# Kernel optimization log

Measured on AMD Instinct MI355X. Metric: run time of the kernel, lower is better.

The kernel has to match this reference:

```python
import jax, jax.numpy as jnp
import numpy as np

LN_EPS = 1e-5

def _layernorm(x, g, b):
    mu = jnp.mean(x, axis=-1, keepdims=True)
    var = jnp.mean(jnp.square(x - mu), axis=-1, keepdims=True)
    return (x - mu) * jax.lax.rsqrt(var + LN_EPS) * g + b

def setup_inputs() -> dict:
    key = jax.random.key(0)
    B, T, C = 8, 2048, 1024
    ks = jax.random.split(key, 16)
    s = 1.0 / np.sqrt(C)
    inp = {
        'x':   jax.random.normal(ks[0], (B, T, C), dtype=jnp.float32),
        'Wq':  jax.random.uniform(ks[1], (C, C), jnp.float32, -s, s),
        'bq':  jax.random.uniform(ks[2], (C,), jnp.float32, -s, s),
        'Wk':  jax.random.uniform(ks[3], (C, C), jnp.float32, -s, s),
        'bk':  jax.random.uniform(ks[4], (C,), jnp.float32, -s, s),
        'Wv':  jax.random.uniform(ks[5], (C, C), jnp.float32, -s, s),
        'bv':  jax.random.uniform(ks[6], (C,), jnp.float32, -s, s),
        'g1':  jnp.ones((C,), jnp.float32),
        'be1': jnp.zeros((C,), jnp.float32),
        'W1':  jax.random.uniform(ks[7], (C, C), jnp.float32, -s, s),
        'bf1': jax.random.uniform(ks[8], (C,), jnp.float32, -s, s),
        'W2':  jax.random.uniform(ks[9], (C, C), jnp.float32, -s, s),
        'bf2': jax.random.uniform(ks[10], (C,), jnp.float32, -s, s),
        'g2':  jnp.ones((C,), jnp.float32),
        'be2': jnp.zeros((C,), jnp.float32),
    }
    return inp

def reference(x, Wq, bq, Wk, bk, Wv, bv, g1, be1, W1, bf1, W2, bf2, g2, be2):
    B, T, C = x.shape
    q = x @ Wq + bq
    k = x @ Wk + bk
    v = x @ Wv + bv
    # FFT cross-correlation along time axis
    fq = jnp.fft.rfft(q, axis=1)
    fk = jnp.fft.rfft(k, axis=1)
    corr = jnp.fft.irfft(fq * jnp.conj(fk), n=T, axis=1)  # [B,T,C]
    weights = jax.nn.softmax(corr, axis=1)
    # einsum 'btd,btv->btd': weights * sum over v's channel dim
    attn = weights * jnp.sum(v, axis=-1, keepdims=True)
    x = _layernorm(x + attn, g1, be1)
    h = jax.nn.relu(x @ W1 + bf1) @ W2 + bf2
    x = _layernorm(x + h, g2, be2)
    return x
```

## Files before the change

kernel.cpp:

```cpp
#include <hip/hip_runtime.h>
#include <math.h>

#define B_DIM 8
#define T_DIM 2048
#define C_DIM 1024
#define BT_DIM (B_DIM * T_DIM)
#define FSZ ((size_t)BT_DIM * C_DIM)
#define LN_EPS 1e-5f

typedef __bf16 bf16x8 __attribute__((ext_vector_type(8)));
typedef _Float16 f16x8 __attribute__((ext_vector_type(8)));
typedef float f32x4 __attribute__((ext_vector_type(4)));

__device__ __forceinline__ unsigned short f2bf(float f) {
  __bf16 h = (__bf16)f;
  return __builtin_bit_cast(unsigned short, h);
}
__device__ __forceinline__ unsigned short f2h(float f) {
  _Float16 h = (_Float16)f;
  return __builtin_bit_cast(unsigned short, h);
}
__device__ __forceinline__ float bf2f(unsigned short u) {
  unsigned int v = ((unsigned int)u) << 16;
  return __builtin_bit_cast(float, v);
}

__device__ __forceinline__ void gld16(const void* g, void* l) {
  __builtin_amdgcn_global_load_lds(
      (const __attribute__((address_space(1))) unsigned int*)g,
      (__attribute__((address_space(3))) unsigned int*)l, 16, 0, 0);
}

__device__ __forceinline__ int swz(int a) {
  return a ^ (((a >> 4) ^ (a >> 8)) & 15);
}

__device__ __forceinline__ int enc11(int f) {
  return ((f & 3) << 9) | (((f >> 2) & 3) << 7) | (((f >> 4) & 3) << 5) |
         (((f >> 6) & 3) << 3) | (((f >> 8) & 3) << 1) | ((f >> 10) & 1);
}

__global__ __launch_bounds__(256)
void cvt_split_sv_kernel(const float* __restrict__ x, const float* __restrict__ wvsum,
                         const float* __restrict__ bvsum,
                         unsigned short* __restrict__ hi, unsigned short* __restrict__ lo,
                         float* __restrict__ sv) {
  const int r = blockIdx.x;
  const int tid = threadIdx.x;
  const size_t base = (size_t)r * C_DIM + (tid << 2);
  float4 v = *(const float4*)(x + base);
  float4 w = *(const float4*)(wvsum + (tid << 2));
  float f[4] = {v.x, v.y, v.z, v.w};
  unsigned short hv[4], lv[4];
#pragma unroll
  for (int i = 0; i < 4; i++) {
    _Float16 hb = (_Float16)f[i];
    hv[i] = __builtin_bit_cast(unsigned short, hb);
    lv[i] = f2h(f[i] - (float)hb);
  }
  *(ushort4*)(hi + base) = make_ushort4(hv[0], hv[1], hv[2], hv[3]);
  *(ushort4*)(lo + base) = make_ushort4(lv[0], lv[1], lv[2], lv[3]);
  float s = v.x * w.x + v.y * w.y + v.z * w.z + v.w * w.w;
#pragma unroll
  for (int off = 32; off > 0; off >>= 1) s += __shfl_down(s, off);
  __shared__ float ps[4];
  if ((tid & 63) == 0) ps[tid >> 6] = s;
  __syncthreads();
  if (tid == 0) sv[r] = ps[0] + ps[1] + ps[2] + ps[3] + bvsum[0];
}

__global__ __launch_bounds__(256)
void wtrans_f16_kernel(const float* __restrict__ W, unsigned short* __restrict__ Wt,
                       int K, int N) {
  __shared__ float tile[32][33];
  const int tid = threadIdx.x;
  const int tx = tid & 31, ty = tid >> 5;
  const int n0 = blockIdx.x * 32, k0 = blockIdx.y * 32;
#pragma unroll
  for (int i = 0; i < 4; i++) {
    int row = ty + i * 8;
    tile[row][tx] = W[(size_t)(k0 + row) * N + n0 + tx];
  }
  __syncthreads();
#pragma unroll
  for (int i = 0; i < 4; i++) {
    int row = ty + i * 8;
    Wt[(size_t)(n0 + row) * K + k0 + tx] = f2h(tile[tx][row]);
  }
}

__global__ __launch_bounds__(256)
void wtrans_kernel(const float* __restrict__ W, unsigned short* __restrict__ Wt,
                   int K, int N) {
  __shared__ float tile[32][33];
  const int tid = threadIdx.x;
  const int tx = tid & 31, ty = tid >> 5;
  const int n0 = blockIdx.x * 32, k0 = blockIdx.y * 32;
#pragma unroll
  for (int i = 0; i < 4; i++) {
    int row = ty + i * 8;
    tile[row][tx] = W[(size_t)(k0 + row) * N + n0 + tx];
  }
  __syncthreads();
#pragma unroll
  for (int i = 0; i < 4; i++) {
    int row = ty + i * 8;
    Wt[(size_t)(n0 + row) * K + k0 + tx] = f2bf(tile[tx][row]);
  }
}

__global__ __launch_bounds__(256)
void wv_rowsum_kernel(const float* __restrict__ Wv, const float* __restrict__ bv,
                      float* __restrict__ wvsum, float* __restrict__ bvsum) {
  const int r = blockIdx.x;
  const int tid = threadIdx.x;
  const float* src = (r < C_DIM) ? (Wv + (size_t)r * C_DIM) : bv;
  float4 t4 = *(const float4*)(src + (tid << 2));
  float s = t4.x + t4.y + t4.z + t4.w;
#pragma unroll
  for (int off = 32; off > 0; off >>= 1) s += __shfl_down(s, off);
  __shared__ float ps[4];
  if ((tid & 63) == 0) ps[tid >> 6] = s;
  __syncthreads();
  if (tid == 0) {
    float v = ps[0] + ps[1] + ps[2] + ps[3];
    if (r < C_DIM) wvsum[r] = v; else bvsum[0] = v;
  }
}

__global__ __launch_bounds__(256, 2)
void gemm_bf16_kernel(const __bf16* __restrict__ A, const __bf16* __restrict__ Bt,
                      const float* __restrict__ bias, float* Yf, unsigned short* Yb,
                      int K, int N, int do_relu) {
  __shared__ __align__(16) __bf16 As[128 * 32];
  __shared__ __align__(16) __bf16 Bs[128 * 32];
  const int tid = threadIdx.x;
  const int wave = tid >> 6, lane = tid & 63;
  const int wr = wave >> 1, wc = wave & 1;
  const int r15 = lane & 15, kq = lane >> 4;
  const int h = blockIdx.y * 8 + blockIdx.x;
  const int xcd = h & 7, s = h >> 3;
  const int mIdx = (xcd << 4) + (s & 7) + ((s >> 6) << 3);
  const int nIdx = (s >> 3) & 7;
  const int m0 = mIdx * 128, n0 = nIdx * 128;

  f32x4 acc[4][4] = {};

  for (int k0 = 0; k0 < K; k0 += 32) {
#pragma unroll
    for (int r = 0; r < 2; ++r) {
      int idx = r * 256 + tid;
      int row = idx >> 2;
      int ko = (idx & 3) ^ ((row >> 1) & 3);
      gld16(A + (size_t)(m0 + row) * K + k0 + ko * 8, &As[idx * 8]);
      gld16(Bt + (size_t)(n0 + row) * K + k0 + ko * 8, &Bs[idx * 8]);
    }
    __syncthreads();
    bf16x8 afr[4], bfr[4];
#pragma unroll
    for (int i = 0; i < 4; i++) {
      int ar = wr * 64 + i * 16 + r15;
      afr[i] = *(const bf16x8*)&As[(ar * 4 + (kq ^ ((ar >> 1) & 3))) * 8];
      int br = wc * 64 + i * 16 + r15;
      bfr[i] = *(const bf16x8*)&Bs[(br * 4 + (kq ^ ((br >> 1) & 3))) * 8];
    }
#pragma unroll
    for (int mi = 0; mi < 4; mi++)
#pragma unroll
      for (int ni = 0; ni < 4; ni++)
        acc[mi][ni] = __builtin_amdgcn_mfma_f32_16x16x32_bf16(afr[mi], bfr[ni], acc[mi][ni], 0, 0, 0);
    __syncthreads();
  }

  float bv[4];
#pragma unroll
  for (int ni = 0; ni < 4; ni++) bv[ni] = bias[n0 + wc * 64 + ni * 16 + r15];

#pragma unroll
  for (int mi = 0; mi < 4; mi++)
#pragma unroll
    for (int ni = 0; ni < 4; ni++) {
      const int n = n0 + wc * 64 + ni * 16 + r15;
#pragma unroll
      for (int r = 0; r < 4; r++) {
        const int m = m0 + wr * 64 + mi * 16 + kq * 4 + r;
        float v = acc[mi][ni][r] + bv[ni];
        if (do_relu) v = fmaxf(v, 0.f);
        if (Yf) Yf[(size_t)m * N + n] = v;
        if (Yb) Yb[(size_t)m * N + n] = f2bf(v);
      }
    }
}

__global__ __launch_bounds__(512, 2)
void gemm_qkT_f16_8ph_kernel(const _Float16* __restrict__ Ahi, const _Float16* __restrict__ Alo,
                             const _Float16* __restrict__ Bq, const _Float16* __restrict__ Bk,
                             const float* __restrict__ biasq, const float* __restrict__ biask,
                             float* __restrict__ Yq, float* __restrict__ Yk, int K, int N) {
  __shared__ __align__(16) _Float16 AhL[3][256 * 32];
  __shared__ __align__(16) _Float16 AlL[3][256 * 32];
  __shared__ __align__(16) _Float16 BqL[3][128 * 32];
  __shared__ __align__(16) _Float16 BkL[3][128 * 32];

  const int tid = threadIdx.x;
  const int wave = tid >> 6, lane = tid & 63;
  const int wr = wave >> 2, wc = wave & 3;
  const int r15 = lane & 15, kq = lane >> 4;
  const int h = blockIdx.y * 8 + blockIdx.x;
  const int xcd = h & 7, s = h >> 3;
  const int mIdx = (xcd << 3) + (s & 3) + ((s >> 5) << 2);
  const int nIdx = (s >> 2) & 7;
  const int m0 = mIdx * 256, n0 = nIdx * 128;
  const int NT = K >> 5;

  const int row_a0 = tid >> 2;
  const int row_a1 = row_a0 + 128;
  const int ch = tid & 3;
  const int ko0 = ch ^ ((row_a0 >> 1) & 3);
  const int ko1 = ch ^ ((row_a1 >> 1) & 3);
  const _Float16* agh0 = Ahi + (size_t)(m0 + row_a0) * K + ko0 * 8;
  const _Float16* agl0 = Alo + (size_t)(m0 + row_a0) * K + ko0 * 8;
  const _Float16* agh1 = Ahi + (size_t)(m0 + row_a1) * K + ko1 * 8;
  const _Float16* agl1 = Alo + (size_t)(m0 + row_a1) * K + ko1 * 8;
  const _Float16* bgq  = Bq  + (size_t)(n0 + row_a0) * K + ko0 * 8;
  const _Float16* bgk  = Bk  + (size_t)(n0 + row_a0) * K + ko0 * 8;

  const int ksel = kq ^ ((r15 >> 1) & 3);
  const int aoff = (wr * 128 + r15) * 32 + ksel * 8;
  const int boff = (wc * 32 + r15) * 32 + ksel * 8;

  f32x4 accq[8][2] = {};
  f32x4 acck[8][2] = {};

  gld16(agh0 + 0, &AhL[0][(size_t)tid * 8]);
  gld16(agl0 + 0, &AlL[0][(size_t)tid * 8]);
  gld16(agh1 + 0, &AhL[0][(size_t)(tid + 512) * 8]);
  gld16(agl1 + 0, &AlL[0][(size_t)(tid + 512) * 8]);
  gld16(bgq + 0, &BqL[0][(size_t)tid * 8]);
  gld16(bgk + 0, &BkL[0][(size_t)tid * 8]);
  gld16(agh0 + 32, &AhL[1][(size_t)tid * 8]);
  gld16(agl0 + 32, &AlL[1][(size_t)tid * 8]);
  gld16(agh1 + 32, &AhL[1][(size_t)(tid + 512) * 8]);
  gld16(agl1 + 32, &AlL[1][(size_t)(tid + 512) * 8]);
  gld16(bgq + 32, &BqL[1][(size_t)tid * 8]);
  gld16(bgk + 32, &BkL[1][(size_t)tid * 8]);

  int bR = 0;
  int bS = 2;

  for (int j = 0; j < NT; ++j) {
    if (j < NT - 1) {
      asm volatile("s_waitcnt vmcnt(6)" ::: "memory");
    } else {
      asm volatile("s_waitcnt vmcnt(0)" ::: "memory");
    }
    __builtin_amdgcn_s_barrier();
    __builtin_amdgcn_sched_barrier(0);

    const int kk = (j + 2) * 32;
    const bool doStage = (j + 2 < NT);

    f16x8 bqf[2], bkf[2];
#pragma unroll
    for (int ni = 0; ni < 2; ++ni) {
      bqf[ni] = *(const f16x8*)&BqL[bR][boff + ni * 512];
      bkf[ni] = *(const f16x8*)&BkL[bR][boff + ni * 512];
    }

#pragma unroll
    for (int p = 0; p < 4; ++p) {
      f16x8 ah0 = *(const f16x8*)&AhL[bR][aoff + (2 * p + 0) * 512];
      f16x8 al0 = *(const f16x8*)&AlL[bR][aoff + (2 * p + 0) * 512];
      f16x8 ah1 = *(const f16x8*)&AhL[bR][aoff + (2 * p + 1) * 512];
      f16x8 al1 = *(const f16x8*)&AlL[bR][aoff + (2 * p + 1) * 512];
      if (doStage) {
        if (p == 0) {
          gld16(agh0 + kk, &AhL[bS][(size_t)tid * 8]);
          gld16(agl0 + kk, &AlL[bS][(size_t)tid * 8]);
        }
        if (p == 1) {
          gld16(agh1 + kk, &AhL[bS][(size_t)(tid + 512) * 8]);
          gld16(agl1 + kk, &AlL[bS][(size_t)(tid + 512) * 8]);
        }
        if (p == 2) gld16(bgq + kk, &BqL[bS][(size_t)tid * 8]);
        if (p == 3) gld16(bgk + kk, &BkL[bS][(size_t)tid * 8]);
      }
      __builtin_amdgcn_s_barrier();
      asm volatile("s_waitcnt lgkmcnt(0)" ::: "memory");
      __builtin_amdgcn_sched_barrier(0);
      __builtin_amdgcn_s_setprio(1);
#pragma unroll
      for (int m2 = 0; m2 < 2; ++m2) {
        const int mi = 2 * p + m2;
        const f16x8 ahv = m2 ? ah1 : ah0;
        const f16x8 alv = m2 ? al1 : al0;
#pragma unroll
        for (int ni = 0; ni < 2; ++ni) {
          accq[mi][ni] = __builtin_amdgcn_mfma_f32_16x16x32_f16(ahv, bqf[ni], accq[mi][ni], 0, 0, 0);
          accq[mi][ni] = __builtin_amdgcn_mfma_f32_16x16x32_f16(alv, bqf[ni], accq[mi][ni], 0, 0, 0);
          acck[mi][ni] = __builtin_amdgcn_mfma_f32_16x16x32_f16(ahv, bkf[ni], acck[mi][ni], 0, 0, 0);
          acck[mi][ni] = __builtin_amdgcn_mfma_f32_16x16x32_f16(alv, bkf[ni], acck[mi][ni], 0, 0, 0);
        }
      }
      __builtin_amdgcn_s_setprio(0);
      __builtin_amdgcn_sched_barrier(0);
    }

    bR = (bR + 1 == 3) ? 0 : bR + 1;
    bS = (bS + 1 == 3) ? 0 : bS + 1;
  }

  float bvq[2], bvk[2];
#pragma unroll
  for (int ni = 0; ni < 2; ++ni) {
    bvq[ni] = biasq[n0 + wc * 32 + ni * 16 + r15];
    bvk[ni] = biask[n0 + wc * 32 + ni * 16 + r15];
  }

#pragma unroll
  for (int mi = 0; mi < 8; ++mi) {
    const int mbase = m0 + wr * 128 + mi * 16 + kq * 4;
    const int bb = mbase >> 11;
    const int t = mbase & (T_DIM - 1);
#pragma unroll
    for (int ni = 0; ni < 2; ++ni) {
      const int n = n0 + wc * 32 + ni * 16 + r15;
      const size_t o = ((size_t)bb * C_DIM + n) * T_DIM + t;
      *(float4*)(Yq + o) = make_float4(accq[mi][ni][0] + bvq[ni], accq[mi][ni][1] + bvq[ni],
                                       accq[mi][ni][2] + bvq[ni], accq[mi][ni][3] + bvq[ni]);
      *(float4*)(Yk + o) = make_float4(acck[mi][ni][0] + bvk[ni], acck[mi][ni][1] + bvk[ni],
                                       acck[mi][ni][2] + bvk[ni], acck[mi][ni][3] + bvk[ni]);
    }
  }
}

__device__ void fft_dif(float2* X, const float2* tw, int tid, float sgn) {
#pragma unroll
  for (int s = 0; s < 5; s++) {
    const int m = 512 >> (2 * s);
    const int jstep = 512 / m;
#pragma unroll
    for (int ii = 0; ii < 2; ii++) {
      const int i = tid + ii * 256;
      const int q = i & (m - 1);
      const int a0 = ((i - q) << 2) + q;
      float2 x0 = X[swz(a0)];
      float2 x1 = X[swz(a0 + m)];
      float2 x2 = X[swz(a0 + 2 * m)];
      float2 x3 = X[swz(a0 + 3 * m)];
      float2 t0 = make_float2(x0.x + x2.x, x0.y + x2.y);
      float2 t2 = make_float2(x0.x - x2.x, x0.y - x2.y);
      float2 t1 = make_float2(x1.x + x3.x, x1.y + x3.y);
      float2 t3 = make_float2(x1.x - x3.x, x1.y - x3.y);
      const float jx = -sgn * t3.y, jy = sgn * t3.x;
      float2 y0 = make_float2(t0.x + t1.x, t0.y + t1.y);
      float2 y1 = make_float2(t2.x + jx, t2.y + jy);
      float2 y2 = make_float2(t0.x - t1.x, t0.y - t1.y);
      float2 y3 = make_float2(t2.x - jx, t2.y - jy);
      const int j1 = q * jstep;
      float2 tv = tw[swz(j1)];
      const float c1 = tv.x, s1 = tv.y * sgn;
      const float c2 = c1 * c1 - s1 * s1, s2 = 2.f * c1 * s1;
      const float c3 = c2 * c1 - s2 * s1, s3 = c2 * s1 + s2 * c1;
      X[swz(a0)] = y0;
      X[swz(a0 + m)] = make_float2(c1 * y1.x - s1 * y1.y, c1 * y1.y + s1 * y1.x);
      X[swz(a0 + 2 * m)] = make_float2(c2 * y2.x - s2 * y2.y, c2 * y2.y + s2 * y2.x);
      X[swz(a0 + 3 * m)] = make_float2(c3 * y3.x - s3 * y3.y, c3 * y3.y + s3 * y3.x);
    }
    __syncthreads();
  }
#pragma unroll
  for (int ii = 0; ii < 4; ii++) {
    const int a = (tid + ii * 256) << 1;
    float2 u = X[swz(a)], v = X[swz(a + 1)];
    X[swz(a)] = make_float2(u.x + v.x, u.y + v.y);
    X[swz(a + 1)] = make_float2(u.x - v.x, u.y - v.y);
  }
  __syncthreads();
}

__device__ void fft_dit_inv(float2* X, const float2* tw, int tid) {
#pragma unroll
  for (int ii = 0; ii < 4; ii++) {
    const int a = (tid + ii * 256) << 1;
    float2 u = X[swz(a)], v = X[swz(a + 1)];
    X[swz(a)] = make_float2(u.x + v.x, u.y + v.y);
    X[swz(a + 1)] = make_float2(u.x - v.x, u.y - v.y);
  }
  __syncthreads();
#pragma unroll
  for (int s = 4; s >= 0; s--) {
    const int m = 512 >> (2 * s);
    const int jstep = 512 / m;
#pragma unroll
    for (int ii = 0; ii < 2; ii++) {
      const int i = tid + ii * 256;
      const int q = i & (m - 1);
      const int a0 = ((i - q) << 2) + q;
      float2 v0 = X[swz(a0)];
      float2 v1 = X[swz(a0 + m)];
      float2 v2 = X[swz(a0 + 2 * m)];
      float2 v3 = X[swz(a0 + 3 * m)];
      const int j1 = q * jstep;
      float2 tv = tw[swz(j1)];
      const float c1 = tv.x, s1 = tv.y;
      const float c2 = c1 * c1 - s1 * s1, s2 = 2.f * c1 * s1;
      const float c3 = c2 * c1 - s2 * s1, s3 = c2 * s1 + s2 * c1;
      float2 w1 = make_float2(c1 * v1.x - s1 * v1.y, c1 * v1.y + s1 * v1.x);
      float2 w2 = make_float2(c2 * v2.x - s2 * v2.y, c2 * v2.y + s2 * v2.x);
      float2 w3 = make_float2(c3 * v3.x - s3 * v3.y, c3 * v3.y + s3 * v3.x);
      float2 t0 = make_float2(v0.x + w2.x, v0.y + w2.y);
      float2 t2 = make_float2(v0.x - w2.x, v0.y - w2.y);
      float2 t1 = make_float2(w1.x + w3.x, w1.y + w3.y);
      float2 t3 = make_float2(w1.x - w3.x, w1.y - w3.y);
      const float jx = -t3.y, jy = t3.x;
      X[swz(a0)] = make_float2(t0.x + t1.x, t0.y + t1.y);
      X[swz(a0 + m)] = make_float2(t2.x + jx, t2.y + jy);
      X[swz(a0 + 2 * m)] = make_float2(t0.x - t1.x, t0.y - t1.y);
      X[swz(a0 + 3 * m)] = make_float2(t2.x - jx, t2.y - jy);
    }
    __syncthreads();
  }
}

__global__ __launch_bounds__(256)
void corr_fft_kernel(const float* qT, const float* kT, unsigned short* __restrict__ wT,
                     float* __restrict__ Iv) {
  __shared__ float2 bA[2048];
  __shared__ float2 bB[2048];
  __shared__ float2 tw[512];
  __shared__ float2 red[4];
  const int tid = threadIdx.x;
  const int wave = tid >> 6, lane = tid & 63;
  const int b = blockIdx.y;
  const int c0 = blockIdx.x * 2;
  const float* q0 = qT + ((size_t)b * C_DIM + c0) * T_DIM;
  const float* k0p = kT + ((size_t)b * C_DIM + c0) * T_DIM;

#pragma unroll
  for (int jj = 0; jj < 2; jj++) {
    int j = tid + jj * 256;
    float sA, cA;
    __sincosf((float)j * (6.283185307179586f / 2048.0f), &sA, &cA);
    tw[swz(j)] = make_float2(cA, sA);
  }

#pragma unroll
  for (int jj = 0; jj < 8; jj++) {
    int t = tid + jj * 256;
    bA[swz(t)] = make_float2(q0[t], q0[t + T_DIM]);
    bB[swz(t)] = make_float2(k0p[t], k0p[t + T_DIM]);
  }
  __syncthreads();

  fft_dif(bA, tw, tid, -1.0f);
  fft_dif(bB, tw, tid, -1.0f);

#pragma unroll 1
  for (int f = tid; f <= 1024; f += 256) {
    const int g = (2048 - f) & 2047;
    const int p = swz(enc11(f));
    const int p2 = swz(enc11(g));
    float2 Zq = bA[p], Zq2 = bA[p2];
    float2 Zk = bB[p], Zk2 = bB[p2];
    float2 Aq = make_float2(0.5f * (Zq.x + Zq2.x), 0.5f * (Zq.y - Zq2.y));
    float2 Dq = make_float2(Zq.x - Zq2.x, Zq.y + Zq2.y);
    float2 Bq = make_float2(0.5f * Dq.y, -0.5f * Dq.x);
    float2 Ak = make_float2(0.5f * (Zk.x + Zk2.x), 0.5f * (Zk.y - Zk2.y));
    float2 Dk = make_float2(Zk.x - Zk2.x, Zk.y + Zk2.y);
    float2 Bk = make_float2(0.5f * Dk.y, -0.5f * Dk.x);
    float2 G = make_float2(Aq.x * Ak.x + Aq.y * Ak.y, Aq.y * Ak.x - Aq.x * Ak.y);
    float2 H = make_float2(Bq.x * Bk.x + Bq.y * Bk.y, Bq.y * Bk.x - Bq.x * Bk.y);
    bA[p] = make_float2(G.x - H.y, G.y + H.x);
    if (p2 != p) bA[p2] = make_float2(G.x + H.y, -G.y + H.x);
  }
  __syncthreads();

  fft_dit_inv(bA, tw, tid);

  unsigned short* o0 = wT + ((size_t)b * C_DIM + c0) * T_DIM;
  const float sc = 1.0f / 2048.0f;
  float mx0 = -INFINITY, mx1 = -INFINITY;
#pragma unroll
  for (int jj = 0; jj < 8; jj++) {
    int t = tid + jj * 256;
    float2 o = bA[swz(t)];
    mx0 = fmaxf(mx0, o.x);
    mx1 = fmaxf(mx1, o.y);
  }
#pragma unroll
  for (int off = 32; off > 0; off >>= 1) {
    mx0 = fmaxf(mx0, __shfl_down(mx0, off));
    mx1 = fmaxf(mx1, __shfl_down(mx1, off));
  }
  if (lane == 0) red[wave] = make_float2(mx0, mx1);
  __syncthreads();
  const float M0 = fmaxf(fmaxf(red[0].x, red[1].x), fmaxf(red[2].x, red[3].x));
  const float M1 = fmaxf(fmaxf(red[0].y, red[1].y), fmaxf(red[2].y, red[3].y));
  __syncthreads();
  float s0 = 0.f, s1 = 0.f;
#pragma unroll
  for (int jj = 0; jj < 8; jj++) {
    int t = tid + jj * 256;
    float2 o = bA[swz(t)];
    float e0 = __expf((o.x - M0) * sc);
    float e1 = __expf((o.y - M1) * sc);
    s0 += e0;
    s1 += e1;
    o0[t] = f2bf(e0);
    o0[t + T_DIM] = f2bf(e1);
  }
#pragma unroll
  for (int off = 32; off > 0; off >>= 1) {
    s0 += __shfl_down(s0, off);
    s1 += __shfl_down(s1, off);
  }
  if (lane == 0) red[wave] = make_float2(s0, s1);
  __syncthreads();
  if (tid == 0) {
    float S0 = red[0].x + red[1].x + red[2].x + red[3].x;
    float S1 = red[0].y + red[1].y + red[2].y + red[3].y;
    Iv[(size_t)b * C_DIM + c0] = 1.0f / S0;
    Iv[(size_t)b * C_DIM + c0 + 1] = 1.0f / S1;
  }
}

__global__ __launch_bounds__(512)
void attn_ln_kernel(const unsigned short* __restrict__ wT, const float* __restrict__ Iv,
                    const float* __restrict__ sv, const float* __restrict__ x,
                    const float* __restrict__ g, const float* __restrict__ be,
                    unsigned short* __restrict__ outb) {
  __shared__ float att[32][1028];
  const int tid = threadIdx.x;
  const int b = blockIdx.y;
  const int t0 = blockIdx.x * 32;

  const int tx = tid & 31;
  const int cy = tid >> 5;
  const unsigned short* cb = wT + (size_t)b * C_DIM * T_DIM + t0 + tx;
  const float* Ib = Iv + (size_t)b * C_DIM;
#pragma unroll 8
  for (int it = 0; it < 64; ++it) {
    const int c = cy + (it << 4);
    att[tx][c] = bf2f(cb[(size_t)c * T_DIM]) * Ib[c];
  }
  __syncthreads();

  const int t = tid >> 4;
  const int l16 = tid & 15;
  const float svv = sv[(size_t)b * T_DIM + t0 + t];
  const float* xr = x + ((size_t)b * T_DIM + t0 + t) * C_DIM;
  float s = 0.f, s2 = 0.f;
#pragma unroll
  for (int j = 0; j < 16; ++j) {
    const int c = (l16 + (j << 4)) << 2;
    float4 xv = *(const float4*)(xr + c);
    float4 av = *(const float4*)&att[t][c];
    float v0 = xv.x + av.x * svv;
    float v1 = xv.y + av.y * svv;
    float v2 = xv.z + av.z * svv;
    float v3 = xv.w + av.w * svv;
    *(float4*)&att[t][c] = make_float4(v0, v1, v2, v3);
    s += v0 + v1 + v2 + v3;
    s2 += v0 * v0 + v1 * v1 + v2 * v2 + v3 * v3;
  }
#pragma unroll
  for (int off = 8; off > 0; off >>= 1) {
    s += __shfl_xor(s, off);
    s2 += __shfl_xor(s2, off);
  }
  const float mu = s * (1.0f / C_DIM);
  const float var = s2 * (1.0f / C_DIM) - mu * mu;
  const float rs = rsqrtf(var + LN_EPS);
  unsigned short* obrow = outb + ((size_t)b * T_DIM + t0 + t) * C_DIM;
#pragma unroll
  for (int j = 0; j < 16; ++j) {
    const int c = (l16 + (j << 4)) << 2;
    float4 val = *(const float4*)&att[t][c];
    float4 gv = *(const float4*)(g + c);
    float4 bev = *(const float4*)(be + c);
    float o0 = (val.x - mu) * rs * gv.x + bev.x;
    float o1 = (val.y - mu) * rs * gv.y + bev.y;
    float o2 = (val.z - mu) * rs * gv.z + bev.z;
    float o3 = (val.w - mu) * rs * gv.w + bev.w;
    *(ushort4*)(obrow + c) = make_ushort4(f2bf(o0), f2bf(o1), f2bf(o2), f2bf(o3));
  }
}

__global__ __launch_bounds__(256)
void add_ln_bf_kernel(const unsigned short* __restrict__ A, const float* __restrict__ Bv,
                      const float* __restrict__ g, const float* __restrict__ be,
                      float* __restrict__ outf) {
  const int r = blockIdx.x;
  const int tid = threadIdx.x;
  const size_t base = (size_t)r * C_DIM + (tid << 2);
  ushort4 a4 = *(const ushort4*)(A + base);
  float4 b = *(const float4*)(Bv + base);
  float x0 = bf2f(a4.x) + b.x;
  float x1 = bf2f(a4.y) + b.y;
  float x2 = bf2f(a4.z) + b.z;
  float x3 = bf2f(a4.w) + b.w;
  float s = x0 + x1 + x2 + x3;
  float s2 = x0 * x0 + x1 * x1 + x2 * x2 + x3 * x3;
#pragma unroll
  for (int off = 32; off > 0; off >>= 1) {
    s += __shfl_down(s, off);
    s2 += __shfl_down(s2, off);
  }
  __shared__ float ps[4], ps2[4];
  if ((tid & 63) == 0) { ps[tid >> 6] = s; ps2[tid >> 6] = s2; }
  __syncthreads();
  float S = ps[0] + ps[1] + ps[2] + ps[3];
  float S2 = ps2[0] + ps2[1] + ps2[2] + ps2[3];
  const float mu = S * (1.0f / C_DIM);
  const float var = S2 * (1.0f / C_DIM) - mu * mu;
  const float rs = rsqrtf(var + LN_EPS);
  float4 gv = *(const float4*)(g + (tid << 2));
  float4 bev = *(const float4*)(be + (tid << 2));
  float o0 = (x0 - mu) * rs * gv.x + bev.x;
  float o1 = (x1 - mu) * rs * gv.y + bev.y;
  float o2 = (x2 - mu) * rs * gv.z + bev.z;
  float o3 = (x3 - mu) * rs * gv.w + bev.w;
  *(float4*)(outf + base) = make_float4(o0, o1, o2, o3);
}

extern "C" void kernel_launch(void* const* d_in, const int* in_sizes, int n_in,
                              void* d_out, int out_size, void* d_ws, size_t ws_size,
                              hipStream_t stream) {
  const float* x   = (const float*)d_in[0];
  const float* Wq  = (const float*)d_in[1];
  const float* bq  = (const float*)d_in[2];
  const float* Wk  = (const float*)d_in[3];
  const float* bk  = (const float*)d_in[4];
  const float* Wv  = (const float*)d_in[5];
  const float* bv  = (const float*)d_in[6];
  const float* g1  = (const float*)d_in[7];
  const float* be1 = (const float*)d_in[8];
  const float* W1  = (const float*)d_in[9];
  const float* bf1 = (const float*)d_in[10];
  const float* W2  = (const float*)d_in[11];
  const float* bf2 = (const float*)d_in[12];
  const float* g2  = (const float*)d_in[13];
  const float* be2 = (const float*)d_in[14];
  float* out = (float*)d_out;

  float* ws = (float*)d_ws;
  float* qbuf = ws;
  float* kbuf = ws + FSZ;
  unsigned short* xhi = (unsigned short*)(ws + 2 * FSZ);
  unsigned short* xlo = xhi + FSZ;
  unsigned short* wA = xlo + FSZ;
  unsigned short* wB = wA + (size_t)C_DIM * C_DIM;
  float* sv = (float*)(wB + (size_t)C_DIM * C_DIM);
  float* wvsum = sv + BT_DIM;
  float* bvsum = wvsum + C_DIM;
  float* Iv = bvsum + 1;

  const dim3 blk(256);
  const dim3 ggrid(C_DIM / 128, BT_DIM / 128);
  const dim3 qkgrid(C_DIM / 128, BT_DIM / 256);
  const dim3 tgrid(C_DIM / 32, C_DIM / 32);

  wv_rowsum_kernel<<<dim3(C_DIM + 1), blk, 0, stream>>>(Wv, bv, wvsum, bvsum);

  cvt_split_sv_kernel<<<dim3(BT_DIM), blk, 0, stream>>>(x, wvsum, bvsum, xhi, xlo, sv);

  wtrans_f16_kernel<<<tgrid, blk, 0, stream>>>(Wq, wA, C_DIM, C_DIM);
  wtrans_f16_kernel<<<tgrid, blk, 0, stream>>>(Wk, wB, C_DIM, C_DIM);
  gemm_qkT_f16_8ph_kernel<<<qkgrid, dim3(512), 0, stream>>>(
      (const _Float16*)xhi, (const _Float16*)xlo,
      (const _Float16*)wA, (const _Float16*)wB,
      bq, bk, qbuf, kbuf, C_DIM, C_DIM);

  corr_fft_kernel<<<dim3(C_DIM / 2, B_DIM), blk, 0, stream>>>(qbuf, kbuf, xlo, Iv);

  attn_ln_kernel<<<dim3(T_DIM / 32, B_DIM), dim3(512), 0, stream>>>(
      xlo, Iv, sv, x, g1, be1, xhi);

  wtrans_kernel<<<tgrid, blk, 0, stream>>>(W1, wA, C_DIM, C_DIM);
  wtrans_kernel<<<tgrid, blk, 0, stream>>>(W2, wB, C_DIM, C_DIM);

  gemm_bf16_kernel<<<ggrid, blk, 0, stream>>>((const __bf16*)xhi, (const __bf16*)wA,
                                              bf1, nullptr, xlo, C_DIM, C_DIM, 1);
  gemm_bf16_kernel<<<ggrid, blk, 0, stream>>>((const __bf16*)xlo, (const __bf16*)wB,
                                              bf2, qbuf, nullptr, C_DIM, C_DIM, 0);

  add_ln_bf_kernel<<<dim3(BT_DIM), blk, 0, stream>>>(xhi, qbuf, g2, be2, out);
}
```

Measured before the change: 517.5 us.

## Pipeline FFN GEMMs with triple-buffered 256x128 tiles and bf16 second output

Replaces the simple double-sync bf16 GEMM used for the two FFN matmuls with a 512-thread, 256x128-tile kernel. It triple-buffers LDS, issues global loads two k-steps ahead, and interleaves them with MFMA phases under explicit waitcnt, barrier and priority control. The second FFN GEMM now writes bf16 instead of fp32, and the final add+LayerNorm reads that bf16 buffer, which halves that intermediate's memory traffic. The cost is extra rounding of the FFN output before the residual add and LayerNorm.

```diff
diff --git a/kernel.cpp b/kernel.cpp
--- a/kernel.cpp
+++ b/kernel.cpp
@@ -128,68 +128,113 @@
   }
 }
 
-__global__ __launch_bounds__(256, 2)
-void gemm_bf16_kernel(const __bf16* __restrict__ A, const __bf16* __restrict__ Bt,
-                      const float* __restrict__ bias, float* Yf, unsigned short* Yb,
-                      int K, int N, int do_relu) {
-  __shared__ __align__(16) __bf16 As[128 * 32];
-  __shared__ __align__(16) __bf16 Bs[128 * 32];
+__global__ __launch_bounds__(512, 4)
+void gemm_bf16_8ph_kernel(const __bf16* __restrict__ A, const __bf16* __restrict__ Bt,
+                          const float* __restrict__ bias, unsigned short* __restrict__ Yb,
+                          int K, int N, int do_relu) {
+  __shared__ __align__(16) __bf16 AsL[3][256 * 32];
+  __shared__ __align__(16) __bf16 BsL[3][128 * 32];
+
   const int tid = threadIdx.x;
   const int wave = tid >> 6, lane = tid & 63;
-  const int wr = wave >> 1, wc = wave & 1;
+  const int wr = wave >> 2, wc = wave & 3;
   const int r15 = lane & 15, kq = lane >> 4;
   const int h = blockIdx.y * 8 + blockIdx.x;
   const int xcd = h & 7, s = h >> 3;
-  const int mIdx = (xcd << 4) + (s & 7) + ((s >> 6) << 3);
-  const int nIdx = (s >> 3) & 7;
-  const int m0 = mIdx * 128, n0 = nIdx * 128;
-
-  f32x4 acc[4][4] = {};
-
-  for (int k0 = 0; k0 < K; k0 += 32) {
-#pragma unroll
-    for (int r = 0; r < 2; ++r) {
-      int idx = r * 256 + tid;
-      int row = idx >> 2;
-      int ko = (idx & 3) ^ ((row >> 1) & 3);
-      gld16(A + (size_t)(m0 + row) * K + k0 + ko * 8, &As[idx * 8]);
-      gld16(Bt + (size_t)(n0 + row) * K + k0 + ko * 8, &Bs[idx * 8]);
-    }
-    __syncthreads();
-    bf16x8 afr[4], bfr[4];
-#pragma unroll
-    for (int i = 0; i < 4; i++) {
-      int ar = wr * 64 + i * 16 + r15;
-      afr[i] = *(const bf16x8*)&As[(ar * 4 + (kq ^ ((ar >> 1) & 3))) * 8];
-      int br = wc * 64 + i * 16 + r15;
-      bfr[i] = *(const bf16x8*)&Bs[(br * 4 + (kq ^ ((br >> 1) & 3))) * 8];
-    }
-#pragma unroll
-    for (int mi = 0; mi < 4; mi++)
-#pragma unroll
-      for (int ni = 0; ni < 4; ni++)
-        acc[mi][ni] = __builtin_amdgcn_mfma_f32_16x16x32_bf16(afr[mi], bfr[ni], acc[mi][ni], 0, 0, 0);
-    __syncthreads();
-  }
-
-  float bv[4];
-#pragma unroll
-  for (int ni = 0; ni < 4; ni++) bv[ni] = bias[n0 + wc * 64 + ni * 16 + r15];
-
-#pragma unroll
-  for (int mi = 0; mi < 4; mi++)
-#pragma unroll
-    for (int ni = 0; ni < 4; ni++) {
-      const int n = n0 + wc * 64 + ni * 16 + r15;
-#pragma unroll
-      for (int r = 0; r < 4; r++) {
-        const int m = m0 + wr * 64 + mi * 16 + kq * 4 + r;
+  const int mIdx = (xcd << 3) + (s & 3) + ((s >> 5) << 2);
+  const int nIdx = (s >> 2) & 7;
+  const int m0 = mIdx * 256, n0 = nIdx * 128;
+  const int NT = K >> 5;
+
+  const int row_a0 = tid >> 2;
+  const int row_a1 = row_a0 + 128;
+  const int ch = tid & 3;
+  const int ko0 = ch ^ ((row_a0 >> 1) & 3);
+  const int ko1 = ch ^ ((row_a1 >> 1) & 3);
+  const __bf16* ag0 = A  + (size_t)(m0 + row_a0) * K + ko0 * 8;
+  const __bf16* ag1 = A  + (size_t)(m0 + row_a1) * K + ko1 * 8;
+  const __bf16* bg  = Bt + (size_t)(n0 + row_a0) * K + ko0 * 8;
+
+  const int ksel = kq ^ ((r15 >> 1) & 3);
+  const int aoff = (wr * 128 + r15) * 32 + ksel * 8;
+  const int boff = (wc * 32 + r15) * 32 + ksel * 8;
+
+  f32x4 acc[8][2] = {};
+
+  gld16(ag0 + 0, &AsL[0][(size_t)tid * 8]);
+  gld16(ag1 + 0, &AsL[0][(size_t)(tid + 512) * 8]);
+  gld16(bg + 0, &BsL[0][(size_t)tid * 8]);
+  gld16(ag0 + 32, &AsL[1][(size_t)tid * 8]);
+  gld16(ag1 + 32, &AsL[1][(size_t)(tid + 512) * 8]);
+  gld16(bg + 32, &BsL[1][(size_t)tid * 8]);
+
+  int bR = 0;
+  int bS = 2;
+
+  for (int j = 0; j < NT; ++j) {
+    if (j < NT - 1) {
+      asm volatile("s_waitcnt vmcnt(3)" ::: "memory");
+    } else {
+      asm volatile("s_waitcnt vmcnt(0)" ::: "memory");
+    }
+    __builtin_amdgcn_s_barrier();
+    __builtin_amdgcn_sched_barrier(0);
+
+    const int kk = (j + 2) * 32;
+    const bool doStage = (j + 2 < NT);
+
+    bf16x8 bf[2];
+#pragma unroll
+    for (int ni = 0; ni < 2; ++ni)
+      bf[ni] = *(const bf16x8*)&BsL[bR][boff + ni * 512];
+
+#pragma unroll
+    for (int p = 0; p < 4; ++p) {
+      bf16x8 a0 = *(const bf16x8*)&AsL[bR][aoff + (2 * p + 0) * 512];
+      bf16x8 a1 = *(const bf16x8*)&AsL[bR][aoff + (2 * p + 1) * 512];
+      if (doStage) {
+        if (p == 0) gld16(ag0 + kk, &AsL[bS][(size_t)tid * 8]);
+        if (p == 1) gld16(ag1 + kk, &AsL[bS][(size_t)(tid + 512) * 8]);
+        if (p == 2) gld16(bg + kk, &BsL[bS][(size_t)tid * 8]);
+      }
+      __builtin_amdgcn_s_barrier();
+      asm volatile("s_waitcnt lgkmcnt(0)" ::: "memory");
+      __builtin_amdgcn_sched_barrier(0);
+      __builtin_amdgcn_s_setprio(1);
+#pragma unroll
+      for (int m2 = 0; m2 < 2; ++m2) {
+        const int mi = 2 * p + m2;
+        const bf16x8 av = m2 ? a1 : a0;
+#pragma unroll
+        for (int ni = 0; ni < 2; ++ni)
+          acc[mi][ni] = __builtin_amdgcn_mfma_f32_16x16x32_bf16(av, bf[ni], acc[mi][ni], 0, 0, 0);
+      }
+      __builtin_amdgcn_s_setprio(0);
+      __builtin_amdgcn_sched_barrier(0);
+    }
+
+    bR = (bR + 1 == 3) ? 0 : bR + 1;
+    bS = (bS + 1 == 3) ? 0 : bS + 1;
+  }
+
+  float bv[2];
+#pragma unroll
+  for (int ni = 0; ni < 2; ++ni) bv[ni] = bias[n0 + wc * 32 + ni * 16 + r15];
+
+#pragma unroll
+  for (int mi = 0; mi < 8; ++mi) {
+    const int mbase = m0 + wr * 128 + mi * 16 + kq * 4;
+#pragma unroll
+    for (int ni = 0; ni < 2; ++ni) {
+      const int n = n0 + wc * 32 + ni * 16 + r15;
+#pragma unroll
+      for (int r = 0; r < 4; ++r) {
         float v = acc[mi][ni][r] + bv[ni];
         if (do_relu) v = fmaxf(v, 0.f);
-        if (Yf) Yf[(size_t)m * N + n] = v;
-        if (Yb) Yb[(size_t)m * N + n] = f2bf(v);
+        Yb[(size_t)(mbase + r) * N + n] = f2bf(v);
       }
     }
+  }
 }
 
 __global__ __launch_bounds__(512, 2)
@@ -588,18 +633,18 @@
 }
 
 __global__ __launch_bounds__(256)
-void add_ln_bf_kernel(const unsigned short* __restrict__ A, const float* __restrict__ Bv,
+void add_ln_bb_kernel(const unsigned short* __restrict__ A, const unsigned short* __restrict__ Bv,
                       const float* __restrict__ g, const float* __restrict__ be,
                       float* __restrict__ outf) {
   const int r = blockIdx.x;
   const int tid = threadIdx.x;
   const size_t base = (size_t)r * C_DIM + (tid << 2);
   ushort4 a4 = *(const ushort4*)(A + base);
-  float4 b = *(const float4*)(Bv + base);
-  float x0 = bf2f(a4.x) + b.x;
-  float x1 = bf2f(a4.y) + b.y;
-  float x2 = bf2f(a4.z) + b.z;
-  float x3 = bf2f(a4.w) + b.w;
+  ushort4 b4 = *(const ushort4*)(Bv + base);
+  float x0 = bf2f(a4.x) + bf2f(b4.x);
+  float x1 = bf2f(a4.y) + bf2f(b4.y);
+  float x2 = bf2f(a4.z) + bf2f(b4.z);
+  float x3 = bf2f(a4.w) + bf2f(b4.w);
   float s = x0 + x1 + x2 + x3;
   float s2 = x0 * x0 + x1 * x1 + x2 * x2 + x3 * x3;
 #pragma unroll
@@ -655,9 +700,9 @@
   float* wvsum = sv + BT_DIM;
   float* bvsum = wvsum + C_DIM;
   float* Iv = bvsum + 1;
+  unsigned short* h2b = (unsigned short*)kbuf;
 
   const dim3 blk(256);
-  const dim3 ggrid(C_DIM / 128, BT_DIM / 128);
   const dim3 qkgrid(C_DIM / 128, BT_DIM / 256);
   const dim3 tgrid(C_DIM / 32, C_DIM / 32);
 
@@ -680,10 +725,10 @@
   wtrans_kernel<<<tgrid, blk, 0, stream>>>(W1, wA, C_DIM, C_DIM);
   wtrans_kernel<<<tgrid, blk, 0, stream>>>(W2, wB, C_DIM, C_DIM);
 
-  gemm_bf16_kernel<<<ggrid, blk, 0, stream>>>((const __bf16*)xhi, (const __bf16*)wA,
-                                              bf1, nullptr, xlo, C_DIM, C_DIM, 1);
-  gemm_bf16_kernel<<<ggrid, blk, 0, stream>>>((const __bf16*)xlo, (const __bf16*)wB,
-                                              bf2, qbuf, nullptr, C_DIM, C_DIM, 0);
-
-  add_ln_bf_kernel<<<dim3(BT_DIM), blk, 0, stream>>>(xhi, qbuf, g2, be2, out);
-}
+  gemm_bf16_8ph_kernel<<<qkgrid, dim3(512), 0, stream>>>(
+      (const __bf16*)xhi, (const __bf16*)wA, bf1, xlo, C_DIM, C_DIM, 1);
+  gemm_bf16_8ph_kernel<<<qkgrid, dim3(512), 0, stream>>>(
+      (const __bf16*)xlo, (const __bf16*)wB, bf2, h2b, C_DIM, C_DIM, 0);
+
+  add_ln_bb_kernel<<<dim3(BT_DIM), blk, 0, stream>>>(xhi, h2b, g2, be2, out);
+}
```

Result: no change. 522.7 us (+1.0%).
